# Performance work log

Hardware: AMD Instinct MI355X
Metric: run time of the kernel (lower is better)

## Reference

```python
import jax, jax.numpy as jnp
import numpy as np

B, F, C = 2, 2, 64          # batch, lookup frames, feature channels (resnet layer1)
D = 96                      # num_depth_bins
HM, WM = 48, 160            # matching resolution = 192x640 // 4
MIN_D, MAX_D = 0.1, 20.0
EPS = 1e-7


def _pix_coords():
    # Homogeneous pixel grid [3, H*W] (BackprojectDepth.pix_coords)
    ys, xs = jnp.meshgrid(jnp.arange(HM, dtype=jnp.float32),
                          jnp.arange(WM, dtype=jnp.float32), indexing='ij')
    return jnp.stack([xs.ravel(), ys.ravel(), jnp.ones(HM * WM, jnp.float32)], 0)


def _bilinear_zeros(img, gx, gy):
    # torch F.grid_sample(mode='bilinear', padding_mode='zeros', align_corners=True)
    # img [C,H,W]; gx,gy are unnormalized pixel coords [Hg,Wg]
    Ci, H, W = img.shape
    x0 = jnp.floor(gx); y0 = jnp.floor(gy)
    wx1 = gx - x0; wy1 = gy - y0
    flat = img.reshape(Ci, H * W)

    def corner(ix, iy, w):
        valid = (ix >= 0) & (ix <= W - 1) & (iy >= 0) & (iy <= H - 1)
        idx = (jnp.clip(iy, 0, H - 1).astype(jnp.int32) * W
               + jnp.clip(ix, 0, W - 1).astype(jnp.int32)).ravel()
        v = flat[:, idx].reshape((Ci,) + gx.shape)
        return v * (w * valid.astype(img.dtype))[None]

    return (corner(x0, y0, (1 - wx1) * (1 - wy1))
            + corner(x0 + 1, y0, wx1 * (1 - wy1))
            + corner(x0, y0 + 1, (1 - wx1) * wy1)
            + corner(x0 + 1, y0 + 1, wx1 * wy1))


def _match_one(current, lookups, poses, K, invK, depth_bins, pix, interior):
    # current [C,H,W]; lookups [F,C,H,W]; poses [F,4,4]; K/invK [4,4]
    # BackprojectDepth: world points for every depth bin
    cam_rays = invK[:3, :3] @ pix                                    # [3,HW]
    pts = depth_bins[:, None, None] * cam_rays[None]                 # [D,3,HW]
    pts = jnp.concatenate([pts, jnp.ones((D, 1, HM * WM), pts.dtype)], 1)  # [D,4,HW]

    def per_frame(feat, T):
        # Project3D: P = K @ T, pix = P[:3] @ pts, normalize by z
        P = (K @ T)[:3]                                              # [3,4]
        cp = jnp.einsum('ij,djk->dik', P, pts)                       # [D,3,HW]
        z = cp[:, 2] + EPS
        px = (cp[:, 0] / z).reshape(D, HM, WM)                       # pixel x coords
        py = (cp[:, 1] / z).reshape(D, HM, WM)
        # (normalizing to [-1,1] then unnormalizing in grid_sample with
        #  align_corners=True is the identity, so we sample at px,py directly)
        warped = jax.vmap(lambda gx, gy: _bilinear_zeros(feat, gx, gy))(px, py)  # [D,C,H,W]
        sx = jax.lax.stop_gradient(px); sy = jax.lax.stop_gradient(py)
        edge = ((sx >= 2.0) & (sx <= WM - 2) & (sy >= 2.0) & (sy <= HM - 2)
                ).astype(jnp.float32) * interior
        valid = (T.sum() != 0).astype(jnp.float32)                   # skip zero poses
        return jnp.abs(warped - current[None]).mean(1) * edge * valid  # [D,H,W]

    diffs = jax.vmap(per_frame)(lookups, poses)                      # [F,D,H,W]
    cost = diffs.sum(0)
    counts = (diffs > 0).astype(jnp.float32).sum(0)
    cost = cost / (counts + EPS)
    cv_feature = jax.lax.stop_gradient(cost)
    missing = (cost == 0).astype(jnp.float32)
    # set_missing_to_max
    cost = cost * (1 - missing) + cost.max(0, keepdims=True) * missing
    return cost, missing, cv_feature


def _forward(current_feats, lookup_feats, poses, K, invK):
    depth_bins = jnp.linspace(MIN_D, MAX_D, D, dtype=jnp.float32)    # linear binning
    pix = _pix_coords()
    interior = jnp.zeros((HM, WM), jnp.float32).at[2:-2, 2:-2].set(1.0)
    return jax.vmap(lambda c, l, p, k, ik: _match_one(
        c, l, p, k, ik, depth_bins, pix, interior))(
        current_feats, lookup_feats, poses, K, invK)


def setup_inputs():
    key = jax.random.key(0)
    k1, k2, k3 = jax.random.split(key, 3)
    current_feats = jax.random.normal(k1, (B, C, HM, WM), jnp.float32)
    lookup_feats = jax.random.normal(k2, (B, F, C, HM, WM), jnp.float32)
    # near-identity relative poses with random translations (realistic ego-motion)
    t = 0.2 * jax.random.normal(k3, (B, F, 3), jnp.float32)
    poses = jnp.broadcast_to(jnp.eye(4, dtype=jnp.float32), (B, F, 4, 4))
    poses = poses.at[..., :3, 3].set(t)
    # KITTI-style intrinsics at matching resolution
    Km = np.eye(4, dtype=np.float32)
    Km[0, 0] = 0.58 * WM; Km[1, 1] = 1.92 * HM
    Km[0, 2] = 0.5 * WM;  Km[1, 2] = 0.5 * HM
    Kmat = jnp.broadcast_to(jnp.asarray(Km), (B, 4, 4))
    invK = jnp.broadcast_to(jnp.asarray(np.linalg.inv(Km)), (B, 4, 4))
    return {"current_feats": current_feats, "lookup_feats": lookup_feats,
            "poses": poses, "K": Kmat, "invK": invK}


def reference(current_feats, lookup_feats, poses, K, invK):
    return _forward(current_feats, lookup_feats, poses, K, invK)
```

## Files before the change

kernel.cpp:

```cpp
#include <hip/hip_runtime.h>
#include <hip/hip_bf16.h>
#include <stdint.h>

#if __has_builtin(__builtin_amdgcn_cvt_pk_f32_fp8) && __has_builtin(__builtin_amdgcn_cvt_pk_fp8_f32)
#define HAS_HW_FP8 1
#else
#define HAS_HW_FP8 0
#include <hip/hip_fp8.h>
#endif

#define B_  2
#define F_  2
#define C_  64
#define D_  96
#define HM_ 48
#define WM_ 160
#define HW_ (HM_ * WM_)
#define NTOT ((size_t)B_ * D_ * HW_)
#define EPS_ 1e-7f
#define DW_  4
#define NDG_ (D_ / DW_)

typedef _Float16 half_t;
typedef _Float16 h2 __attribute__((ext_vector_type(2)));
typedef float f2 __attribute__((ext_vector_type(2)));
typedef unsigned int u32;

struct H4 { h2 a, b; };


__device__ __forceinline__ u32 pk4_fp8(float a, float b, float c, float d) {
#if HAS_HW_FP8
    int r = __builtin_amdgcn_cvt_pk_fp8_f32(a, b, 0, false);
    r = __builtin_amdgcn_cvt_pk_fp8_f32(c, d, r, true);
    return (u32)r;
#else
    __hip_fp8_e4m3 qa(a), qb(b), qc(c), qd(d);
    return (u32)qa.__x | ((u32)qb.__x << 8) | ((u32)qc.__x << 16) |
           ((u32)qd.__x << 24);
#endif
}

template <bool HI>
__device__ __forceinline__ f2 fp8pk(u32 v) {
#if HAS_HW_FP8
    return __builtin_amdgcn_cvt_pk_f32_fp8((int)v, HI);
#else
    u32 w = HI ? (v >> 16) : v;
    __hip_fp8_e4m3 q0, q1;
    q0.__x = (uint8_t)(w & 0xff);
    q1.__x = (uint8_t)((w >> 8) & 0xff);
    f2 r; r.x = (float)q0; r.y = (float)q1;
    return r;
#endif
}

#define NQBLK4 ((B_ * F_ * (C_/4) * (HW_/4)) / 256)
#define NCBLK  ((B_ * (C_/4) * HW_) / 256)

__global__ __launch_bounds__(256) void pack_and_setup(
    const float* __restrict__ look,
    const float* __restrict__ cur,
    uint4* __restrict__ quad4,
    H4* __restrict__ cur2,
    const float* __restrict__ poses,
    const float* __restrict__ K,
    float* __restrict__ Pout,
    float* __restrict__ validOut)
{
    if (blockIdx.x == 0 && threadIdx.x < 64) {
        int t = threadIdx.x;
        if (t < B_ * F_ * 12) {
            int j  = t & 3;
            int i  = (t >> 2) % 3;
            int bf = t / 12;
            int b  = bf / F_;
            const float* Kb = K + (size_t)b * 16;
            const float* T  = poses + (size_t)bf * 16;
            float s = 0.f;
            #pragma unroll
            for (int k = 0; k < 4; ++k) s += Kb[i * 4 + k] * T[k * 4 + j];
            Pout[bf * 12 + i * 4 + j] = s;
        }
        if (t < B_ * F_) {
            const float* T = poses + (size_t)t * 16;
            float s = 0.f;
            #pragma unroll
            for (int k = 0; k < 16; ++k) s += T[k];
            validOut[t] = (s != 0.0f) ? 1.0f : 0.0f;
        }
    }

    int blk = blockIdx.x;
    if (blk < NQBLK4) {
        int t   = blk * 256 + threadIdx.x;
        int g   = t % (HW_ / 4);
        int rem = t / (HW_ / 4);
        int c4  = rem % (C_ / 4);
        int n   = rem / (C_ / 4);
        int x0 = (g * 4) % WM_;
        int y  = (g * 4) / WM_;
        int y1 = min(y + 1, HM_ - 1);
        int xe = min(x0 + 4, WM_ - 1);

        const float* base = look + ((size_t)n * C_ + 4 * c4) * HW_;
        float4 rA[4], rB[4];
        float  eA[4], eB[4];
        #pragma unroll
        for (int k = 0; k < 4; ++k) {
            const float* bc = base + (size_t)k * HW_;
            rA[k] = *(const float4*)(bc + y  * WM_ + x0);
            eA[k] = bc[y  * WM_ + xe];
            rB[k] = *(const float4*)(bc + y1 * WM_ + x0);
            eB[k] = bc[y1 * WM_ + xe];
        }
        const float* fA[4] = {(const float*)&rA[0], (const float*)&rA[1],
                              (const float*)&rA[2], (const float*)&rA[3]};
        const float* fB[4] = {(const float*)&rB[0], (const float*)&rB[1],
                              (const float*)&rB[2], (const float*)&rB[3]};

        uint4* outp = quad4 + ((size_t)(n * (C_ / 4) + c4)) * HW_ + g * 4;
        #pragma unroll
        for (int j = 0; j < 4; ++j) {
            float p01_0 = (j < 3) ? fA[0][j + 1] : eA[0];
            float p01_1 = (j < 3) ? fA[1][j + 1] : eA[1];
            float p01_2 = (j < 3) ? fA[2][j + 1] : eA[2];
            float p01_3 = (j < 3) ? fA[3][j + 1] : eA[3];
            float p11_0 = (j < 3) ? fB[0][j + 1] : eB[0];
            float p11_1 = (j < 3) ? fB[1][j + 1] : eB[1];
            float p11_2 = (j < 3) ? fB[2][j + 1] : eB[2];
            float p11_3 = (j < 3) ? fB[3][j + 1] : eB[3];
            uint4 q;
            q.x = pk4_fp8(fA[0][j], fA[1][j], fA[2][j], fA[3][j]);
            q.y = pk4_fp8(p01_0,    p01_1,    p01_2,    p01_3);
            q.z = pk4_fp8(fB[0][j], fB[1][j], fB[2][j], fB[3][j]);
            q.w = pk4_fp8(p11_0,    p11_1,    p11_2,    p11_3);
            outp[j] = q;
        }
    } else {
        int t   = (blk - NQBLK4) * 256 + threadIdx.x;
        int pix = t % HW_;
        int rem = t / HW_;
        int c4  = rem % (C_ / 4);
        int b   = rem / (C_ / 4);
        const float* p = cur + ((size_t)b * C_ + 4 * c4) * HW_ + pix;
        H4 h;
        h.a = h2{(half_t)(-p[0]),               (half_t)(-p[(size_t)HW_])};
        h.b = h2{(half_t)(-p[2 * (size_t)HW_]), (half_t)(-p[3 * (size_t)HW_])};
        cur2[t] = h;
    }
}

__global__ __launch_bounds__(256) void cost_volume(
    const uint4* __restrict__ quad4,
    const H4* __restrict__ cur2,
    const float* __restrict__ invK,
    const float* __restrict__ P,
    const float* __restrict__ validF,
    float* __restrict__ cvOut)
{
    int blk  = blockIdx.x;
    int tile = blk / (B_ * NDG_);
    int r    = blk % (B_ * NDG_);
    int b    = r / NDG_;
    int dg   = r % NDG_;
    int wave = threadIdx.x >> 6;
    int lane = threadIdx.x & 63;
    int d    = dg * DW_ + wave;
    int hw   = tile * 64 + lane;

    int x = hw % WM_, y = hw / WM_;
    float fx = (float)x, fy = (float)y;

    const float* ik = invK + (size_t)b * 16;
    float rx = ik[0] * fx + ik[1] * fy + ik[2];
    float ry = ik[4] * fx + ik[5] * fy + ik[6];
    float rz = ik[8] * fx + ik[9] * fy + ik[10];

    float depth = 0.1f + (float)d * (19.9f / 95.0f);
    float qx = depth * rx, qy = depth * ry, qz = depth * rz;

    bool inter = (x >= 2 && x <= WM_ - 3 && y >= 2 && y <= HM_ - 3);

    unsigned pixc[F_];
    float wf[F_][4];
    float ff[F_];

    #pragma unroll
    for (int f = 0; f < F_; ++f) {
        const float* Pf = P + (size_t)(b * F_ + f) * 12;
        float cp0 = Pf[0] * qx + Pf[1] * qy + Pf[2]  * qz + Pf[3];
        float cp1 = Pf[4] * qx + Pf[5] * qy + Pf[6]  * qz + Pf[7];
        float cp2 = Pf[8] * qx + Pf[9] * qy + Pf[10] * qz + Pf[11];
        float z  = cp2 + EPS_;
        float gx = cp0 / z, gy = cp1 / z;

        float x0f = floorf(gx), y0f = floorf(gy);
        float wx1 = gx - x0f, wy1 = gy - y0f;
        float wx0 = 1.f - wx1, wy0 = 1.f - wy1;

        int x0 = (int)x0f, y0 = (int)y0f;
        int cx = min(max(x0, 0), WM_ - 1);
        int cy = min(max(y0, 0), HM_ - 1);
        pixc[f] = (unsigned)(cy * WM_ + cx);

        wf[f][0] = wx0 * wy0;
        wf[f][1] = wx1 * wy0;
        wf[f][2] = wx0 * wy1;
        wf[f][3] = wx1 * wy1;

        bool e = (gx >= 2.f) && (gx <= (float)(WM_ - 2)) &&
                 (gy >= 2.f) && (gy <= (float)(HM_ - 2)) && inter;
        ff[f] = (e ? 1.f : 0.f) * validF[b * F_ + f];
    }

    size_t oidx = ((size_t)(b * D_ + d)) * HW_ + hw;

    if (__ballot(ff[0] > 0.f || ff[1] > 0.f) == 0ull) {
        cvOut[oidx] = 0.f;
        return;
    }

    f2 W00_0 = f2{wf[0][0], wf[0][0]}, W01_0 = f2{wf[0][1], wf[0][1]};
    f2 W10_0 = f2{wf[0][2], wf[0][2]}, W11_0 = f2{wf[0][3], wf[0][3]};
    f2 W00_1 = f2{wf[1][0], wf[1][0]}, W01_1 = f2{wf[1][1], wf[1][1]};
    f2 W10_1 = f2{wf[1][2], wf[1][2]}, W11_1 = f2{wf[1][3], wf[1][3]};

    const char* qbp = (const char*)quad4;
    const char* cbp = (const char*)cur2;
    unsigned oA = ((u32)((b * F_ + 0) * (C_ / 4)) * HW_ + pixc[0]) * 16u;
    unsigned oB = ((u32)((b * F_ + 1) * (C_ / 4)) * HW_ + pixc[1]) * 16u;
    unsigned oc = ((u32)(b * (C_ / 4)) * HW_ + (u32)hw) * 8u;

    f2 sA = f2{0.f, 0.f}, sB = f2{0.f, 0.f};

    #pragma unroll 4
    for (int c4i = 0; c4i < C_ / 4; ++c4i) {
        uint4 qa = *(const uint4*)(qbp + oA); oA += (u32)HW_ * 16u;
        uint4 qb = *(const uint4*)(qbp + oB); oB += (u32)HW_ * 16u;
        H4 cu = *(const H4*)(cbp + oc); oc += (u32)HW_ * 8u;

        f2 nc01; nc01.x = (float)cu.a.x; nc01.y = (float)cu.a.y;
        f2 nc23; nc23.x = (float)cu.b.x; nc23.y = (float)cu.b.y;

        f2 a01 = fp8pk<false>(qa.x) * W00_0 + (fp8pk<false>(qa.y) * W01_0 +
                 (fp8pk<false>(qa.z) * W10_0 + (fp8pk<false>(qa.w) * W11_0 + nc01)));
        f2 a23 = fp8pk<true >(qa.x) * W00_0 + (fp8pk<true >(qa.y) * W01_0 +
                 (fp8pk<true >(qa.z) * W10_0 + (fp8pk<true >(qa.w) * W11_0 + nc23)));
        f2 b01 = fp8pk<false>(qb.x) * W00_1 + (fp8pk<false>(qb.y) * W01_1 +
                 (fp8pk<false>(qb.z) * W10_1 + (fp8pk<false>(qb.w) * W11_1 + nc01)));
        f2 b23 = fp8pk<true >(qb.x) * W00_1 + (fp8pk<true >(qb.y) * W01_1 +
                 (fp8pk<true >(qb.z) * W10_1 + (fp8pk<true >(qb.w) * W11_1 + nc23)));

        sA.x += fabsf(a01.x); sA.y += fabsf(a01.y);
        sA.x += fabsf(a23.x); sA.y += fabsf(a23.y);
        sB.x += fabsf(b01.x); sB.y += fabsf(b01.y);
        sB.x += fabsf(b23.x); sB.y += fabsf(b23.y);
    }

    float s0 = sA.x + sA.y;
    float s1 = sB.x + sB.y;

    float m0 = s0 * (1.0f / 64.0f) * ff[0];
    float m1 = s1 * (1.0f / 64.0f) * ff[1];
    float costsum = m0 + m1;
    float counts  = ((m0 > 0.f) ? 1.f : 0.f) + ((m1 > 0.f) ? 1.f : 0.f);
    float scale = (counts > 1.5f) ? (1.0f / (2.0f + EPS_)) : (1.0f / (1.0f + EPS_));
    cvOut[oidx] = costsum * scale;
}

#define FDS_ 4
#define FDP_ (D_ / FDS_)

__global__ __launch_bounds__(256) void finalize(
    const float* __restrict__ cv,
    float* __restrict__ cost,
    float* __restrict__ missing)
{
    int slice = threadIdx.x >> 6;
    int lp    = threadIdx.x & 63;
    int p     = blockIdx.x * 64 + lp;
    int b = p / HW_, hw = p % HW_;
    const float* src = cv + (size_t)b * D_ * HW_ + (size_t)slice * FDP_ * HW_ + hw;

    float v[FDP_];
    float mx = 0.f;
    #pragma unroll
    for (int i = 0; i < FDP_; ++i) {
        v[i] = src[(size_t)i * HW_];
        mx = fmaxf(mx, v[i]);
    }

    __shared__ float lmax[FDS_][64];
    lmax[slice][lp] = mx;
    __syncthreads();
    mx = fmaxf(fmaxf(lmax[0][lp], lmax[1][lp]),
               fmaxf(lmax[2][lp], lmax[3][lp]));

    size_t obase = (size_t)b * D_ * HW_ + (size_t)slice * FDP_ * HW_ + hw;
    #pragma unroll
    for (int i = 0; i < FDP_; ++i) {
        float val = v[i];
        float m = (val == 0.f) ? 1.f : 0.f;
        size_t o = obase + (size_t)i * HW_;
        cost[o]    = (m != 0.f) ? mx : val;
        missing[o] = m;
    }
}

extern "C" void kernel_launch(void* const* d_in, const int* in_sizes, int n_in,
                              void* d_out, int out_size, void* d_ws, size_t ws_size,
                              hipStream_t stream)
{
    const float* current = (const float*)d_in[0];
    const float* lookup  = (const float*)d_in[1];
    const float* poses   = (const float*)d_in[2];
    const float* K       = (const float*)d_in[3];
    const float* invK    = (const float*)d_in[4];

    float* out = (float*)d_out;
    float* costOut    = out;
    float* missingOut = out + NTOT;
    float* cvOut      = out + 2 * NTOT;

    float* ws     = (float*)d_ws;
    float* Pmat   = ws;
    float* validF = Pmat + B_ * F_ * 12;
    uint4* quad4  = (uint4*)(ws + 64);

    H4* cur2 = (H4*)costOut;

    const int npack = NQBLK4 + NCBLK;
    hipLaunchKernelGGL(pack_and_setup, dim3(npack), dim3(256), 0, stream,
                       lookup, current, quad4, cur2, poses, K, Pmat, validF);

    const int nblocks = (HW_ / 64) * B_ * NDG_;
    hipLaunchKernelGGL(cost_volume, dim3(nblocks), dim3(256), 0, stream,
                       quad4, cur2, invK, Pmat, validF, cvOut);

    const int nfin = (B_ * HW_) / 64;
    hipLaunchKernelGGL(finalize, dim3(nfin), dim3(256), 0, stream,
                       cvOut, costOut, missingOut);
}
```

Baseline: 59.63 us.

## Compute bilinear cost in packed fp16 with fp8-to-f16 converts and fdot2 reduction

The cost-volume inner loop now converts fp8 lookup features directly to packed fp16, does the bilinear blend and abs in packed half arithmetic, and reduces each group of 8 channels into an fp32 accumulator with fdot2. The current-frame features are repacked as 8 channels per 16-byte load instead of 4 per 8 bytes, and the loop handles two channel quads per iteration. The goal is to halve the VALU work and cut load instruction count in the compute-bound loop. The cost is that intermediate sums are held in fp16, which loses precision and may hurt accuracy.

```diff
diff --git a/kernel.cpp b/kernel.cpp
--- a/kernel.cpp
+++ b/kernel.cpp
@@ -7,6 +7,12 @@
 #else
 #define HAS_HW_FP8 0
 #include <hip/hip_fp8.h>
+#endif
+
+#if __has_builtin(__builtin_amdgcn_cvt_pk_f16_fp8)
+#define HAS_F16_FP8 1
+#else
+#define HAS_F16_FP8 0
 #endif
 
 #define B_  2
@@ -26,7 +32,7 @@
 typedef float f2 __attribute__((ext_vector_type(2)));
 typedef unsigned int u32;
 
-struct H4 { h2 a, b; };
+struct CH8 { h2 c01, c23, c45, c67; };
 
 
 __device__ __forceinline__ u32 pk4_fp8(float a, float b, float c, float d) {
@@ -42,7 +48,7 @@
 }
 
 template <bool HI>
-__device__ __forceinline__ f2 fp8pk(u32 v) {
+__device__ __forceinline__ f2 fp8pk_f32(u32 v) {
 #if HAS_HW_FP8
     return __builtin_amdgcn_cvt_pk_f32_fp8((int)v, HI);
 #else
@@ -55,14 +61,41 @@
 #endif
 }
 
+template <bool HI>
+__device__ __forceinline__ h2 fp8pk_f16(u32 v) {
+#if HAS_F16_FP8
+    return __builtin_amdgcn_cvt_pk_f16_fp8((int)v, HI);
+#else
+    f2 f = fp8pk_f32<HI>(v);
+    return h2{(half_t)f.x, (half_t)f.y};
+#endif
+}
+
+__device__ __forceinline__ h2 pabs(h2 v) {
+    u32 u; __builtin_memcpy(&u, &v, 4);
+    u &= 0x7FFF7FFFu;
+    h2 r; __builtin_memcpy(&r, &u, 4);
+    return r;
+}
+
+#if __has_builtin(__builtin_amdgcn_fdot2)
+__device__ __forceinline__ float FDOT2(h2 a, h2 b, float c) {
+    return __builtin_amdgcn_fdot2(a, b, c, false);
+}
+#else
+__device__ __forceinline__ float FDOT2(h2 a, h2 b, float c) {
+    return (float)a.x * (float)b.x + (float)a.y * (float)b.y + c;
+}
+#endif
+
 #define NQBLK4 ((B_ * F_ * (C_/4) * (HW_/4)) / 256)
-#define NCBLK  ((B_ * (C_/4) * HW_) / 256)
+#define NCBLK8 ((B_ * (C_/8) * HW_) / 256)
 
 __global__ __launch_bounds__(256) void pack_and_setup(
     const float* __restrict__ look,
     const float* __restrict__ cur,
     uint4* __restrict__ quad4,
-    H4* __restrict__ cur2,
+    CH8* __restrict__ cur8,
     const float* __restrict__ poses,
     const float* __restrict__ K,
     float* __restrict__ Pout,
@@ -141,19 +174,21 @@
         int t   = (blk - NQBLK4) * 256 + threadIdx.x;
         int pix = t % HW_;
         int rem = t / HW_;
-        int c4  = rem % (C_ / 4);
-        int b   = rem / (C_ / 4);
-        const float* p = cur + ((size_t)b * C_ + 4 * c4) * HW_ + pix;
-        H4 h;
-        h.a = h2{(half_t)(-p[0]),               (half_t)(-p[(size_t)HW_])};
-        h.b = h2{(half_t)(-p[2 * (size_t)HW_]), (half_t)(-p[3 * (size_t)HW_])};
-        cur2[t] = h;
+        int c8  = rem % (C_ / 8);
+        int b   = rem / (C_ / 8);
+        const float* p = cur + ((size_t)b * C_ + 8 * c8) * HW_ + pix;
+        CH8 h;
+        h.c01 = h2{(half_t)(-p[0]),               (half_t)(-p[(size_t)HW_])};
+        h.c23 = h2{(half_t)(-p[2 * (size_t)HW_]), (half_t)(-p[3 * (size_t)HW_])};
+        h.c45 = h2{(half_t)(-p[4 * (size_t)HW_]), (half_t)(-p[5 * (size_t)HW_])};
+        h.c67 = h2{(half_t)(-p[6 * (size_t)HW_]), (half_t)(-p[7 * (size_t)HW_])};
+        cur8[t] = h;
     }
 }
 
 __global__ __launch_bounds__(256) void cost_volume(
     const uint4* __restrict__ quad4,
-    const H4* __restrict__ cur2,
+    const CH8* __restrict__ cur8,
     const float* __restrict__ invK,
     const float* __restrict__ P,
     const float* __restrict__ validF,
@@ -221,45 +256,80 @@
         return;
     }
 
-    f2 W00_0 = f2{wf[0][0], wf[0][0]}, W01_0 = f2{wf[0][1], wf[0][1]};
-    f2 W10_0 = f2{wf[0][2], wf[0][2]}, W11_0 = f2{wf[0][3], wf[0][3]};
-    f2 W00_1 = f2{wf[1][0], wf[1][0]}, W01_1 = f2{wf[1][1], wf[1][1]};
-    f2 W10_1 = f2{wf[1][2], wf[1][2]}, W11_1 = f2{wf[1][3], wf[1][3]};
+    h2 W00_0 = h2{(half_t)wf[0][0], (half_t)wf[0][0]};
+    h2 W01_0 = h2{(half_t)wf[0][1], (half_t)wf[0][1]};
+    h2 W10_0 = h2{(half_t)wf[0][2], (half_t)wf[0][2]};
+    h2 W11_0 = h2{(half_t)wf[0][3], (half_t)wf[0][3]};
+    h2 W00_1 = h2{(half_t)wf[1][0], (half_t)wf[1][0]};
+    h2 W01_1 = h2{(half_t)wf[1][1], (half_t)wf[1][1]};
+    h2 W10_1 = h2{(half_t)wf[1][2], (half_t)wf[1][2]};
+    h2 W11_1 = h2{(half_t)wf[1][3], (half_t)wf[1][3]};
 
     const char* qbp = (const char*)quad4;
-    const char* cbp = (const char*)cur2;
+    const char* cbp = (const char*)cur8;
     unsigned oA = ((u32)((b * F_ + 0) * (C_ / 4)) * HW_ + pixc[0]) * 16u;
     unsigned oB = ((u32)((b * F_ + 1) * (C_ / 4)) * HW_ + pixc[1]) * 16u;
-    unsigned oc = ((u32)(b * (C_ / 4)) * HW_ + (u32)hw) * 8u;
-
-    f2 sA = f2{0.f, 0.f}, sB = f2{0.f, 0.f};
-
-    #pragma unroll 4
-    for (int c4i = 0; c4i < C_ / 4; ++c4i) {
-        uint4 qa = *(const uint4*)(qbp + oA); oA += (u32)HW_ * 16u;
-        uint4 qb = *(const uint4*)(qbp + oB); oB += (u32)HW_ * 16u;
-        H4 cu = *(const H4*)(cbp + oc); oc += (u32)HW_ * 8u;
-
-        f2 nc01; nc01.x = (float)cu.a.x; nc01.y = (float)cu.a.y;
-        f2 nc23; nc23.x = (float)cu.b.x; nc23.y = (float)cu.b.y;
-
-        f2 a01 = fp8pk<false>(qa.x) * W00_0 + (fp8pk<false>(qa.y) * W01_0 +
-                 (fp8pk<false>(qa.z) * W10_0 + (fp8pk<false>(qa.w) * W11_0 + nc01)));
-        f2 a23 = fp8pk<true >(qa.x) * W00_0 + (fp8pk<true >(qa.y) * W01_0 +
-                 (fp8pk<true >(qa.z) * W10_0 + (fp8pk<true >(qa.w) * W11_0 + nc23)));
-        f2 b01 = fp8pk<false>(qb.x) * W00_1 + (fp8pk<false>(qb.y) * W01_1 +
-                 (fp8pk<false>(qb.z) * W10_1 + (fp8pk<false>(qb.w) * W11_1 + nc01)));
-        f2 b23 = fp8pk<true >(qb.x) * W00_1 + (fp8pk<true >(qb.y) * W01_1 +
-                 (fp8pk<true >(qb.z) * W10_1 + (fp8pk<true >(qb.w) * W11_1 + nc23)));
-
-        sA.x += fabsf(a01.x); sA.y += fabsf(a01.y);
-        sA.x += fabsf(a23.x); sA.y += fabsf(a23.y);
-        sB.x += fabsf(b01.x); sB.y += fabsf(b01.y);
-        sB.x += fabsf(b23.x); sB.y += fabsf(b23.y);
-    }
-
-    float s0 = sA.x + sA.y;
-    float s1 = sB.x + sB.y;
+    unsigned oc = ((u32)(b * (C_ / 8)) * HW_ + (u32)hw) * 16u;
+
+    const h2 ones = h2{(half_t)1.f, (half_t)1.f};
+    float s0 = 0.f, s1 = 0.f;
+
+    #pragma unroll 2
+    for (int g = 0; g < 8; ++g) {
+        uint4 qa0 = *(const uint4*)(qbp + oA);
+        uint4 qa1 = *(const uint4*)(qbp + oA + (u32)HW_ * 16u);
+        oA += (u32)HW_ * 32u;
+        uint4 qb0 = *(const uint4*)(qbp + oB);
+        uint4 qb1 = *(const uint4*)(qbp + oB + (u32)HW_ * 16u);
+        oB += (u32)HW_ * 32u;
+        CH8 cu = *(const CH8*)(cbp + oc); oc += (u32)HW_ * 16u;
+
+        h2 t, hA, hB;
+
+        t = fp8pk_f16<false>(qa0.w) * W11_0 + cu.c01;
+        t = fp8pk_f16<false>(qa0.z) * W10_0 + t;
+        t = fp8pk_f16<false>(qa0.y) * W01_0 + t;
+        t = fp8pk_f16<false>(qa0.x) * W00_0 + t;
+        hA = pabs(t);
+        t = fp8pk_f16<true>(qa0.w) * W11_0 + cu.c23;
+        t = fp8pk_f16<true>(qa0.z) * W10_0 + t;
+        t = fp8pk_f16<true>(qa0.y) * W01_0 + t;
+        t = fp8pk_f16<true>(qa0.x) * W00_0 + t;
+        hA += pabs(t);
+        t = fp8pk_f16<false>(qa1.w) * W11_0 + cu.c45;
+        t = fp8pk_f16<false>(qa1.z) * W10_0 + t;
+        t = fp8pk_f16<false>(qa1.y) * W01_0 + t;
+        t = fp8pk_f16<false>(qa1.x) * W00_0 + t;
+        hA += pabs(t);
+        t = fp8pk_f16<true>(qa1.w) * W11_0 + cu.c67;
+        t = fp8pk_f16<true>(qa1.z) * W10_0 + t;
+        t = fp8pk_f16<true>(qa1.y) * W01_0 + t;
+        t = fp8pk_f16<true>(qa1.x) * W00_0 + t;
+        hA += pabs(t);
+        s0 = FDOT2(hA, ones, s0);
+
+        t = fp8pk_f16<false>(qb0.w) * W11_1 + cu.c01;
+        t = fp8pk_f16<false>(qb0.z) * W10_1 + t;
+        t = fp8pk_f16<false>(qb0.y) * W01_1 + t;
+        t = fp8pk_f16<false>(qb0.x) * W00_1 + t;
+        hB = pabs(t);
+        t = fp8pk_f16<true>(qb0.w) * W11_1 + cu.c23;
+        t = fp8pk_f16<true>(qb0.z) * W10_1 + t;
+        t = fp8pk_f16<true>(qb0.y) * W01_1 + t;
+        t = fp8pk_f16<true>(qb0.x) * W00_1 + t;
+        hB += pabs(t);
+        t = fp8pk_f16<false>(qb1.w) * W11_1 + cu.c45;
+        t = fp8pk_f16<false>(qb1.z) * W10_1 + t;
+        t = fp8pk_f16<false>(qb1.y) * W01_1 + t;
+        t = fp8pk_f16<false>(qb1.x) * W00_1 + t;
+        hB += pabs(t);
+        t = fp8pk_f16<true>(qb1.w) * W11_1 + cu.c67;
+        t = fp8pk_f16<true>(qb1.z) * W10_1 + t;
+        t = fp8pk_f16<true>(qb1.y) * W01_1 + t;
+        t = fp8pk_f16<true>(qb1.x) * W00_1 + t;
+        hB += pabs(t);
+        s1 = FDOT2(hB, ones, s1);
+    }
 
     float m0 = s0 * (1.0f / 64.0f) * ff[0];
     float m1 = s1 * (1.0f / 64.0f) * ff[1];
@@ -328,15 +398,15 @@
     float* validF = Pmat + B_ * F_ * 12;
     uint4* quad4  = (uint4*)(ws + 64);
 
-    H4* cur2 = (H4*)costOut;
-
-    const int npack = NQBLK4 + NCBLK;
+    CH8* cur8 = (CH8*)costOut;
+
+    const int npack = NQBLK4 + NCBLK8;
     hipLaunchKernelGGL(pack_and_setup, dim3(npack), dim3(256), 0, stream,
-                       lookup, current, quad4, cur2, poses, K, Pmat, validF);
+                       lookup, current, quad4, cur8, poses, K, Pmat, validF);
 
     const int nblocks = (HW_ / 64) * B_ * NDG_;
     hipLaunchKernelGGL(cost_volume, dim3(nblocks), dim3(256), 0, stream,
-                       quad4, cur2, invK, Pmat, validF, cvOut);
+                       quad4, cur8, invK, Pmat, validF, cvOut);
 
     const int nfin = (B_ * HW_) / 64;
     hipLaunchKernelGGL(finalize, dim3(nfin), dim3(256), 0, stream,
```

Result: slower. 61.99 us (+4.0%).
